# Optimization experiments

Hardware: AMD Instinct MI355X
Metric: run time of the kernel (lower is better)

The kernel has to match this reference:

```python
import jax, jax.numpy as jnp
import numpy as np

B, T, F, H = 256, 256, 128, 512


def setup_inputs() -> dict:
    key = jax.random.key(0)
    ks = jax.random.split(key, 16)
    values = jax.random.normal(ks[0], (B, T, F), dtype=jnp.float32)
    masks = (jax.random.uniform(ks[1], (B, T, F)) < 0.7).astype(jnp.float32)
    deltas = jax.random.uniform(ks[2], (B, T, F), dtype=jnp.float32) * 5.0
    empirical_mean = jax.random.normal(ks[3], (F,), dtype=jnp.float32)
    X_filledLOCF = jax.random.normal(ks[4], (B, T, F), dtype=jnp.float32)
    # TemporalDecay params: temp_decay_x is diag (F->F, diagonal weight), temp_decay_h is full (F->H)
    sF = 1.0 / np.sqrt(F)
    wx_diag = jax.random.uniform(ks[5], (F,), minval=-sF, maxval=sF, dtype=jnp.float32)
    bx = jax.random.uniform(ks[6], (F,), minval=-sF, maxval=sF, dtype=jnp.float32)
    Wh = jax.random.uniform(ks[7], (H, F), minval=-sF, maxval=sF, dtype=jnp.float32)
    bh = jax.random.uniform(ks[8], (H,), minval=-sF, maxval=sF, dtype=jnp.float32)
    # GRUCell params, torch layout: weight_ih [3H, 2F+H], weight_hh [3H, H], gate order r,z,n
    sH = 1.0 / np.sqrt(H)
    in_dim = 2 * F + H
    W_ih = jax.random.uniform(ks[9], (3 * H, in_dim), minval=-sH, maxval=sH, dtype=jnp.float32)
    W_hh = jax.random.uniform(ks[10], (3 * H, H), minval=-sH, maxval=sH, dtype=jnp.float32)
    b_ih = jax.random.uniform(ks[11], (3 * H,), minval=-sH, maxval=sH, dtype=jnp.float32)
    b_hh = jax.random.uniform(ks[12], (3 * H,), minval=-sH, maxval=sH, dtype=jnp.float32)
    return {"values": values, "masks": masks, "deltas": deltas,
            "empirical_mean": empirical_mean, "X_filledLOCF": X_filledLOCF,
            "wx_diag": wx_diag, "bx": bx, "Wh": Wh, "bh": bh,
            "W_ih": W_ih, "W_hh": W_hh, "b_ih": b_ih, "b_hh": b_hh}


def _grud_scan(values, masks, deltas, empirical_mean, X_filledLOCF,
               wx_diag, bx, Wh, bh, W_ih, W_hh, b_ih, b_hh):
    Hd = Wh.shape[0]
    h0 = jnp.zeros((values.shape[0], Hd), dtype=values.dtype)

    def step(h, xt):
        x, m, d, x_locf = xt  # each [B, F]
        gamma_h = jnp.exp(-jax.nn.relu(d @ Wh.T + bh))          # [B, H]
        gamma_x = jnp.exp(-jax.nn.relu(d * wx_diag + bx))       # [B, F] (diag TemporalDecay)
        h = h * gamma_h
        x_h = gamma_x * x_locf + (1.0 - gamma_x) * empirical_mean
        x_rep = m * x + (1.0 - m) * x_h
        inp = jnp.concatenate([x_rep, h, m], axis=1)            # [B, 2F+H]
        gi = inp @ W_ih.T + b_ih                                # [B, 3H]
        gh = h @ W_hh.T + b_hh                                  # [B, 3H]
        i_r, i_z, i_n = jnp.split(gi, 3, axis=1)
        h_r, h_z, h_n = jnp.split(gh, 3, axis=1)
        r = jax.nn.sigmoid(i_r + h_r)
        z = jax.nn.sigmoid(i_z + h_z)
        n = jnp.tanh(i_n + r * h_n)
        h_new = (1.0 - z) * n + z * h
        return h_new, h_new

    # time-major for scan: [T, B, F]
    xs = (values.transpose(1, 0, 2), masks.transpose(1, 0, 2),
          deltas.transpose(1, 0, 2), X_filledLOCF.transpose(1, 0, 2))
    h_last, hs = jax.lax.scan(step, h0, xs)
    return hs.transpose(1, 0, 2), h_last  # [B, T, H], [B, H]


def reference(values, masks, deltas, empirical_mean, X_filledLOCF,
              wx_diag, bx, Wh, bh, W_ih, W_hh, b_ih, b_hh):
    return _grud_scan(values, masks, deltas, empirical_mean, X_filledLOCF,
                      wx_diag, bx, Wh, bh, W_ih, W_hh, b_ih, b_hh)
```

## Files before the change

### kernel.cpp

```cpp
#include <hip/hip_runtime.h>
#include <math.h>

#define Bb 256
#define Tt 256
#define Ff 128
#define Hh 512
#define KTOT 768
#define NC 2048

typedef unsigned short u16;
typedef unsigned int   u32;
typedef unsigned long long u64;
typedef __attribute__((ext_vector_type(8))) short s8v;
typedef __attribute__((ext_vector_type(4))) float f4v;
typedef __attribute__((ext_vector_type(4))) u32  u32x4;

#define OFF_GAMMA 0ull
#define OFF_XREP  (OFF_GAMMA + 67108864ull)
#define OFF_MBF   (OFF_XREP  + 16777216ull)
#define OFF_WFRAG (OFF_MBF   + 16777216ull)
#define OFF_BIASC (OFF_WFRAG + 3145728ull)
#define OFF_BAR   (OFF_BIASC + 8192ull)

__device__ __forceinline__ u16 f2b(float x) {
    u32 u = __float_as_uint(x);
    return (u16)((u + 0x7FFFu + ((u >> 16) & 1u)) >> 16);
}
__device__ __forceinline__ float b2f(u16 b) {
    return __uint_as_float(((u32)b) << 16);
}

__global__ __launch_bounds__(256) void k_zero(int* p, int n) {
    int i = blockIdx.x * 256 + threadIdx.x;
    if (i < n) p[i] = 0;
}

__device__ __forceinline__ float xrep_one(float x, float m, float d, float l,
                                          float w, float bb, float em) {
    float gx = expf(-fmaxf(d * w + bb, 0.f));
    float xh = gx * l + (1.f - gx) * em;
    return m * x + (1.f - m) * xh;
}

__global__ __launch_bounds__(256) void k_prep(const float* __restrict__ values,
                                              const float* __restrict__ masks,
                                              const float* __restrict__ deltas,
                                              const float* __restrict__ locf,
                                              const float* __restrict__ emean,
                                              const float* __restrict__ wx,
                                              const float* __restrict__ bxp,
                                              u16* __restrict__ xrep,
                                              u16* __restrict__ mbf) {
    int idx = blockIdx.x * 256 + threadIdx.x;
    int e = idx * 4;
    int f = e & 127;
    float4 xv = *(const float4*)&values[e];
    float4 mv = *(const float4*)&masks[e];
    float4 dv = *(const float4*)&deltas[e];
    float4 lv = *(const float4*)&locf[e];
    float4 wv = *(const float4*)&wx[f];
    float4 bv = *(const float4*)&bxp[f];
    float4 ev = *(const float4*)&emean[f];
    u16 o[4], mo[4];
    o[0] = f2b(xrep_one(xv.x, mv.x, dv.x, lv.x, wv.x, bv.x, ev.x));
    o[1] = f2b(xrep_one(xv.y, mv.y, dv.y, lv.y, wv.y, bv.y, ev.y));
    o[2] = f2b(xrep_one(xv.z, mv.z, dv.z, lv.z, wv.z, bv.z, ev.z));
    o[3] = f2b(xrep_one(xv.w, mv.w, dv.w, lv.w, wv.w, bv.w, ev.w));
    mo[0] = f2b(mv.x); mo[1] = f2b(mv.y); mo[2] = f2b(mv.z); mo[3] = f2b(mv.w);
    *(uint2*)&xrep[e] = *(uint2*)o;
    *(uint2*)&mbf[e]  = *(uint2*)mo;
}

__global__ __launch_bounds__(256) void k_wcomb(const float* __restrict__ W_ih,
                                               const float* __restrict__ W_hh,
                                               const float* __restrict__ b_ih,
                                               const float* __restrict__ b_hh,
                                               u16* __restrict__ wfrag,
                                               float* __restrict__ biasc) {
    int G = blockIdx.x * 256 + threadIdx.x;
    int lane = G & 63;
    int q = G >> 6;
    int ki = q % 24; q /= 24;
    int nt = q & 1;  q >>= 1;
    int wv = q & 3;  q >>= 2;
    int bx = q;
    int c = bx * 128 + wv * 32 + nt * 16 + (lane & 15);
    int kbase = ki * 32 + (lane >> 4) * 8;
    int g = c & 3, jH = c >> 2;
    u16 o[8];
#pragma unroll
    for (int j = 0; j < 8; ++j) {
        int k = kbase + j;
        float w;
        if (g < 3) {
            w = W_ih[(size_t)(g * Hh + jH) * KTOT + k];
            if (g < 2 && k >= Ff && k < Ff + Hh) w += W_hh[(size_t)(g * Hh + jH) * Hh + (k - Ff)];
        } else {
            w = (k >= Ff && k < Ff + Hh) ? W_hh[(size_t)(2 * Hh + jH) * Hh + (k - Ff)] : 0.f;
        }
        o[j] = f2b(w);
    }
    *(uint4*)&wfrag[(size_t)G * 8] = *(uint4*)o;
    if (ki == 0 && (lane >> 4) == 0) {
        float bv;
        if (g == 0)      bv = b_ih[jH] + b_hh[jH];
        else if (g == 1) bv = b_ih[Hh + jH] + b_hh[Hh + jH];
        else if (g == 2) bv = b_ih[2 * Hh + jH];
        else             bv = b_hh[2 * Hh + jH];
        biasc[c] = bv;
    }
}

__global__ __launch_bounds__(256) void k_gamma(const float* __restrict__ deltas,
                                               const float* __restrict__ Wh,
                                               const float* __restrict__ bh,
                                               u16* __restrict__ gamma) {
    __shared__ float A_s[64][68];
    __shared__ float B_s[64][68];
    int tid = threadIdx.x;
    int tx = tid & 15, ty = tid >> 4;
    int bt0 = blockIdx.x * 64;
    int c0  = blockIdx.y * 64;

    float acc[4][4];
#pragma unroll
    for (int i = 0; i < 4; ++i)
#pragma unroll
        for (int j = 0; j < 4; ++j) acc[i][j] = 0.f;

    for (int kc = 0; kc < 2; ++kc) {
#pragma unroll
        for (int s = 0; s < 4; ++s) {
            int v = tid + s * 256;
            int row = v >> 4, c4 = v & 15, kk = c4 * 4;
            int bt = bt0 + row;
            int b = bt & 255, tt = bt >> 8;
            float4 a = *(const float4*)&deltas[b * (Tt * Ff) + tt * Ff + kc * 64 + kk];
            *(float4*)&A_s[row][kk] = a;
        }
#pragma unroll
        for (int s = 0; s < 4; ++s) {
            int v = tid + s * 256;
            int col = v >> 4, c4 = v & 15, kk = c4 * 4;
            float4 w = *(const float4*)&Wh[(c0 + col) * Ff + kc * 64 + kk];
            *(float4*)&B_s[col][kk] = w;
        }
        __syncthreads();
#pragma unroll
        for (int kk = 0; kk < 64; kk += 4) {
            float4 a[4], b[4];
#pragma unroll
            for (int i = 0; i < 4; ++i) a[i] = *(const float4*)&A_s[4 * ty + i][kk];
#pragma unroll
            for (int j = 0; j < 4; ++j) b[j] = *(const float4*)&B_s[4 * tx + j][kk];
#pragma unroll
            for (int i = 0; i < 4; ++i)
#pragma unroll
                for (int j = 0; j < 4; ++j) {
                    acc[i][j] += a[i].x * b[j].x;
                    acc[i][j] += a[i].y * b[j].y;
                    acc[i][j] += a[i].z * b[j].z;
                    acc[i][j] += a[i].w * b[j].w;
                }
        }
        __syncthreads();
    }
#pragma unroll
    for (int i = 0; i < 4; ++i) {
        int bt = bt0 + 4 * ty + i;
        u16 o[4];
#pragma unroll
        for (int j = 0; j < 4; ++j) {
            int col = c0 + 4 * tx + j;
            float x = acc[i][j] + bh[col];
            o[j] = f2b(expf(-fmaxf(x, 0.f)));
        }
        *(uint2*)&gamma[(size_t)bt * Hh + c0 + 4 * tx] = *(uint2*)o;
    }
}

__global__ __launch_bounds__(512, 2) void k_scan(const u16* __restrict__ xrep,
                                                 const u16* __restrict__ mbf,
                                                 const u16* __restrict__ gamma,
                                                 const u16* __restrict__ wfrag,
                                                 const float* __restrict__ biasc,
                                                 int* __restrict__ bar,
                                                 float* __restrict__ hs,
                                                 float* __restrict__ hlast) {
    __shared__ u16  A_s[24 * 64 * 8];
    __shared__ float E_s[16][132];

    int tid = threadIdx.x;
    int lane = tid & 63, w = tid >> 6;

    int L = blockIdx.x + 16 * blockIdx.y;
    int by = (L & 7) + 8 * (L >> 7);
    int bx = (L >> 3) & 15;
    int r0 = by * 16;

    u32x4 Bf[24];
    const u32x4* wf4 = (const u32x4*)wfrag;
#pragma unroll
    for (int ki = 0; ki < 24; ++ki)
        Bf[ki] = wf4[(size_t)(((bx * 8 + w) * 24 + ki) * 64 + lane)];
#pragma unroll
    for (int ki = 0; ki < 24; ++ki)
        asm volatile("" : "+v"(Bf[ki]));

    int srow = lane & 15;
    int koff = (lane >> 4) * 8;

    int bl = tid >> 5, jh = tid & 31;
    int eb = r0 + bl;
    int JH = bx * 32 + jh;
    float4 bi = *(const float4*)&biasc[JH * 4];
    float hreg = 0.f;

    {
        if (w < 4) {
            int kb = w * 32 + koff;
            *(uint4*)&A_s[tid * 8] =
                *(const uint4*)&xrep[(size_t)(r0 + srow) * (Tt * Ff) + 0 * Ff + kb];
        } else {
            int kb = (w - 4) * 32 + koff;
            *(uint4*)&A_s[(tid + 1024) * 8] =
                *(const uint4*)&mbf[(size_t)(r0 + srow) * (Tt * Ff) + 0 * Ff + kb];
        }
        uint4 z; z.x = 0; z.y = 0; z.z = 0; z.w = 0;
#pragma unroll
        for (int e = 0; e < 2; ++e) {
            int ki = 4 + 8 * e + w;
            *(uint4*)&A_s[(ki * 64 + lane) * 8] = z;
        }
    }
    __syncthreads();

    for (int t = 0; t < Tt; ++t) {
        f4v acc = {0.f, 0.f, 0.f, 0.f};
#pragma unroll
        for (int ki = 0; ki < 24; ++ki) {
            s8v a = *(const s8v*)&A_s[(ki * 64 + lane) * 8];
            acc = __builtin_amdgcn_mfma_f32_16x16x32_bf16(a, __builtin_bit_cast(s8v, Bf[ki]), acc, 0, 0, 0);
        }

        {
            int colb = w * 16 + (lane & 15);
            int rq = (lane >> 4) * 4;
#pragma unroll
            for (int r = 0; r < 4; ++r)
                E_s[rq + r][colb] = acc[r];
        }
        __syncthreads();

        uint4 g4[2];
        u16 gdec = 0;
        if (t < Tt - 1) {
            if (w < 4) {
                int kb = w * 32 + koff;
                *(uint4*)&A_s[tid * 8] =
                    *(const uint4*)&xrep[(size_t)(r0 + srow) * (Tt * Ff) + (t + 1) * Ff + kb];
            } else {
                int kb = (w - 4) * 32 + koff;
                *(uint4*)&A_s[(tid + 1024) * 8] =
                    *(const uint4*)&mbf[(size_t)(r0 + srow) * (Tt * Ff) + (t + 1) * Ff + kb];
            }
#pragma unroll
            for (int e = 0; e < 2; ++e) {
                int ki = 4 + 8 * e + w;
                int kh = (ki - 4) * 32 + koff;
                g4[e] = *(const uint4*)&gamma[((size_t)(t + 1) * Bb + (r0 + srow)) * Hh + kh];
            }
            gdec = gamma[((size_t)(t + 1) * Bb + eb) * Hh + JH];
        }

        float4 p = *(const float4*)&E_s[bl][jh * 4];
        float rg = 1.f / (1.f + expf(-(p.x + bi.x)));
        float zz = 1.f / (1.f + expf(-(p.y + bi.y)));
        float nn = tanhf(p.z + bi.z + rg * (p.w + bi.w));
        float hn = (1.f - zz) * nn + zz * hreg;

        __hip_atomic_exchange((u32*)&hs[(size_t)eb * (Tt * Hh) + (size_t)t * Hh + JH],
                              __float_as_uint(hn), __ATOMIC_RELAXED,
                              __HIP_MEMORY_SCOPE_AGENT);

        if (t < Tt - 1) {
            hreg = hn * b2f(gdec);

            asm volatile("s_waitcnt vmcnt(0)" ::: "memory");
            __syncthreads();
            if (tid == 0) {
                int* c = &bar[by * 32];
                __hip_atomic_fetch_add(c, 1, __ATOMIC_RELAXED, __HIP_MEMORY_SCOPE_AGENT);
                int target = 16 * (t + 1);
                int iters = 0;
                while (__hip_atomic_fetch_add(c, 0, __ATOMIC_RELAXED,
                                              __HIP_MEMORY_SCOPE_AGENT) < target) {
                    __builtin_amdgcn_s_sleep(1);
                    if (++iters > (1 << 22)) break;
                }
            }
            __syncthreads();

            float4 hb[4];
#pragma unroll
            for (int e = 0; e < 2; ++e) {
                int ki = 4 + 8 * e + w;
                int kh = (ki - 4) * 32 + koff;
                const float* hp = &hs[(size_t)(r0 + srow) * (Tt * Hh) + (size_t)t * Hh + kh];
                hb[2 * e]     = *(const float4*)hp;
                hb[2 * e + 1] = *(const float4*)(hp + 4);
            }
#pragma unroll
            for (int e = 0; e < 2; ++e) {
                int ki = 4 + 8 * e + w;
                float4 h0 = hb[2 * e];
                float4 h1 = hb[2 * e + 1];
                u16 g8[8];
                *(uint4*)g8 = g4[e];
                u16 o[8];
                o[0] = f2b(h0.x * b2f(g8[0])); o[1] = f2b(h0.y * b2f(g8[1]));
                o[2] = f2b(h0.z * b2f(g8[2])); o[3] = f2b(h0.w * b2f(g8[3]));
                o[4] = f2b(h1.x * b2f(g8[4])); o[5] = f2b(h1.y * b2f(g8[5]));
                o[6] = f2b(h1.z * b2f(g8[6])); o[7] = f2b(h1.w * b2f(g8[7]));
                *(uint4*)&A_s[(ki * 64 + lane) * 8] = *(uint4*)o;
            }
            __syncthreads();
        } else {
            hlast[eb * Hh + JH] = hn;
        }
    }
}

extern "C" void kernel_launch(void* const* d_in, const int* in_sizes, int n_in,
                              void* d_out, int out_size, void* d_ws, size_t ws_size,
                              hipStream_t stream) {
    const float* values = (const float*)d_in[0];
    const float* masks  = (const float*)d_in[1];
    const float* deltas = (const float*)d_in[2];
    const float* emean  = (const float*)d_in[3];
    const float* locf   = (const float*)d_in[4];
    const float* wx     = (const float*)d_in[5];
    const float* bxp    = (const float*)d_in[6];
    const float* Wh     = (const float*)d_in[7];
    const float* bh     = (const float*)d_in[8];
    const float* W_ih   = (const float*)d_in[9];
    const float* W_hh   = (const float*)d_in[10];
    const float* b_ih   = (const float*)d_in[11];
    const float* b_hh   = (const float*)d_in[12];

    char* wsb   = (char*)d_ws;
    u16*  gamma = (u16*)(wsb + OFF_GAMMA);
    u16*  xrep  = (u16*)(wsb + OFF_XREP);
    u16*  mbf   = (u16*)(wsb + OFF_MBF);
    u16*  wfrag = (u16*)(wsb + OFF_WFRAG);
    float* biasc = (float*)(wsb + OFF_BIASC);
    int*  bar   = (int*)(wsb + OFF_BAR);
    float* hs    = (float*)d_out;
    float* hlast = hs + (size_t)Bb * Tt * Hh;

    k_zero<<<2, 256, 0, stream>>>(bar, 512);
    k_prep<<<(Bb * Tt * Ff / 4) / 256, 256, 0, stream>>>(values, masks, deltas, locf,
                                                         emean, wx, bxp, xrep, mbf);
    k_gamma<<<dim3((Tt * Bb) / 64, Hh / 64), 256, 0, stream>>>(deltas, Wh, bh, gamma);
    k_wcomb<<<(NC * KTOT / 8) / 256, 256, 0, stream>>>(W_ih, W_hh, b_ih, b_hh, wfrag, biasc);

    k_scan<<<dim3(16, 16), 512, 0, stream>>>(xrep, mbf, gamma, wfrag, biasc,
                                             bar, hs, hlast);
}
```

Measured before the change: 1.683 ms.

## Replace atomic-counter barrier with per-block flags and overlap input MFMAs with wait

Replaces the single shared atomic counter per row group with one flag slot per block, written with an exchange and polled in parallel by 16 lanes of wave 0 using __all. The input-dependent MFMA slices for the next step (x_rep and mask k-blocks) are computed before waiting on the barrier, so that work overlaps the inter-block synchronisation. The hidden-state output store is packed into 64-bit atomic exchanges by pairing adjacent lanes. The barrier buffer grows and the zeroing launch is enlarged to match.

Measured after the change: 1.663 ms. No clear change (-1.2%).

```diff
diff --git a/kernel.cpp b/kernel.cpp
--- a/kernel.cpp
+++ b/kernel.cpp
@@ -235,10 +235,17 @@
     }
     __syncthreads();
 
+    f4v acc = {0.f, 0.f, 0.f, 0.f};
+#pragma unroll
+    for (int s = 0; s < 8; ++s) {
+        int ki = (s < 4) ? s : (16 + s);
+        s8v a = *(const s8v*)&A_s[(ki * 64 + lane) * 8];
+        acc = __builtin_amdgcn_mfma_f32_16x16x32_bf16(a, __builtin_bit_cast(s8v, Bf[ki]), acc, 0, 0, 0);
+    }
+
     for (int t = 0; t < Tt; ++t) {
-        f4v acc = {0.f, 0.f, 0.f, 0.f};
-#pragma unroll
-        for (int ki = 0; ki < 24; ++ki) {
+#pragma unroll
+        for (int ki = 4; ki < 20; ++ki) {
             s8v a = *(const s8v*)&A_s[(ki * 64 + lane) * 8];
             acc = __builtin_amdgcn_mfma_f32_16x16x32_bf16(a, __builtin_bit_cast(s8v, Bf[ki]), acc, 0, 0, 0);
         }
@@ -279,24 +286,43 @@
         float nn = tanhf(p.z + bi.z + rg * (p.w + bi.w));
         float hn = (1.f - zz) * nn + zz * hreg;
 
-        __hip_atomic_exchange((u32*)&hs[(size_t)eb * (Tt * Hh) + (size_t)t * Hh + JH],
-                              __float_as_uint(hn), __ATOMIC_RELAXED,
-                              __HIP_MEMORY_SCOPE_AGENT);
+        float hn_hi = __shfl_down(hn, 1);
+        if ((jh & 1) == 0) {
+            union { float f[2]; u64 u; } pk;
+            pk.f[0] = hn; pk.f[1] = hn_hi;
+            __hip_atomic_exchange((u64*)&hs[(size_t)eb * (Tt * Hh) + (size_t)t * Hh + JH],
+                                  pk.u, __ATOMIC_RELAXED, __HIP_MEMORY_SCOPE_AGENT);
+        }
 
         if (t < Tt - 1) {
             hreg = hn * b2f(gdec);
 
             asm volatile("s_waitcnt vmcnt(0)" ::: "memory");
             __syncthreads();
-            if (tid == 0) {
-                int* c = &bar[by * 32];
-                __hip_atomic_fetch_add(c, 1, __ATOMIC_RELAXED, __HIP_MEMORY_SCOPE_AGENT);
-                int target = 16 * (t + 1);
+
+            int target = t + 1;
+            if (tid == 0)
+                __hip_atomic_exchange(&bar[by * 512 + bx * 32], target,
+                                      __ATOMIC_RELAXED, __HIP_MEMORY_SCOPE_AGENT);
+
+            f4v acc2 = {0.f, 0.f, 0.f, 0.f};
+#pragma unroll
+            for (int s = 0; s < 8; ++s) {
+                int ki = (s < 4) ? s : (16 + s);
+                s8v a = *(const s8v*)&A_s[(ki * 64 + lane) * 8];
+                acc2 = __builtin_amdgcn_mfma_f32_16x16x32_bf16(a, __builtin_bit_cast(s8v, Bf[ki]), acc2, 0, 0, 0);
+            }
+
+            if (w == 0) {
                 int iters = 0;
-                while (__hip_atomic_fetch_add(c, 0, __ATOMIC_RELAXED,
-                                              __HIP_MEMORY_SCOPE_AGENT) < target) {
+                while (true) {
+                    int v = target;
+                    if (lane < 16)
+                        v = __hip_atomic_fetch_add(&bar[by * 512 + lane * 32], 0,
+                                                   __ATOMIC_RELAXED, __HIP_MEMORY_SCOPE_AGENT);
+                    if (__all(v >= target)) break;
                     __builtin_amdgcn_s_sleep(1);
-                    if (++iters > (1 << 22)) break;
+                    if (++iters > (1 << 20)) break;
                 }
             }
             __syncthreads();
@@ -325,6 +351,7 @@
                 *(uint4*)&A_s[(ki * 64 + lane) * 8] = *(uint4*)o;
             }
             __syncthreads();
+            acc = acc2;
         } else {
             hlast[eb * Hh + JH] = hn;
         }
@@ -358,7 +385,7 @@
     float* hs    = (float*)d_out;
     float* hlast = hs + (size_t)Bb * Tt * Hh;
 
-    k_zero<<<2, 256, 0, stream>>>(bar, 512);
+    k_zero<<<32, 256, 0, stream>>>(bar, 16 * 512);
     k_prep<<<(Bb * Tt * Ff / 4) / 256, 256, 0, stream>>>(values, masks, deltas, locf,
                                                          emean, wx, bxp, xrep, mbf);
     k_gamma<<<dim3((Tt * Bb) / 64, Hh / 64), 256, 0, stream>>>(deltas, Wh, bh, gamma);
```
